# Optimization experiments

Hardware: AMD Instinct MI355X
Metric: run time of the kernel (lower is better)

## Reference

```python
import jax, jax.numpy as jnp
import numpy as np

B, S, H, NH = 2, 384, 768, 12
DPH = H // NH
SCALE = 1.0 / np.sqrt(DPH)


def _layer_norm(x, g, b, eps=1e-6):
    m = jnp.mean(x, axis=-1, keepdims=True)
    v = jnp.mean(jnp.square(x - m), axis=-1, keepdims=True)
    return (x - m) * jax.lax.rsqrt(v + eps) * g + b


def setup_inputs() -> dict:
    key = jax.random.key(0)
    ks = jax.random.split(key, 12)
    std = 0.02
    return {
        "hidden_states": jax.random.normal(ks[0], (B, S, H), jnp.float32),
        "attention_mask": jnp.ones((B, S), jnp.int32),
        "rel_pos_embedding": jax.random.normal(ks[1], (B, S, S, H), jnp.float32),
        "Wq": jax.random.normal(ks[2], (H, H), jnp.float32) * std,
        "bq": jnp.zeros((H,), jnp.float32),
        "Wk": jax.random.normal(ks[3], (H, H), jnp.float32) * std,
        "bk": jnp.zeros((H,), jnp.float32),
        "Wv": jax.random.normal(ks[4], (H, H), jnp.float32) * std,
        "bv": jnp.zeros((H,), jnp.float32),
        "Wr": jax.random.normal(ks[5], (H, H), jnp.float32) * std,
        "br": jnp.zeros((H,), jnp.float32),
        "u": jax.random.normal(ks[6], (NH, DPH), jnp.float32) * std,
        "v": jax.random.normal(ks[7], (NH, DPH), jnp.float32) * std,
        "Wf": jax.random.normal(ks[8], (H, H), jnp.float32) * std,
        "bf": jnp.zeros((H,), jnp.float32),
        "ln_g": jnp.ones((H,), jnp.float32),
        "ln_b": jnp.zeros((H,), jnp.float32),
    }


def reference(hidden_states, attention_mask, rel_pos_embedding,
              Wq, bq, Wk, bk, Wv, bv, Wr, br, u, v, Wf, bf, ln_g, ln_b):
    # projections (torch Linear: x @ W.T + b)
    def heads(x):  # [B,S,H] -> [B,NH,S,DPH]
        return x.reshape(B, S, NH, DPH).transpose(0, 2, 1, 3)
    q = heads(hidden_states @ Wq.T + bq)
    k = heads(hidden_states @ Wk.T + bk)
    val = heads(hidden_states @ Wv.T + bv)
    # relative embedding projection: [B,S,S,H] -> [B,S,S,NH,DPH]
    rel = (rel_pos_embedding @ Wr.T + br).reshape(B, S, S, NH, DPH)

    # Transformer-XL style decomposition
    AC = jnp.einsum('bhid,bhjd->bhij', q + u[None, :, None, :], k)
    Bp = jnp.einsum('bhid,bijhd->bhij', q, rel)
    Dp = jnp.einsum('hd,bijhd->bhij', v, rel)
    scores = (AC + Bp + Dp) * SCALE

    # 2-D mask -> [B,1,1,S]
    ext = (1.0 - attention_mask[:, None, None, :].astype(scores.dtype)) * (-1e18)
    probs = jax.nn.softmax(scores + ext, axis=-1)  # dropout is identity at eval

    ctx = jnp.einsum('bhij,bhjd->bhid', probs, val)
    ctx = ctx.transpose(0, 2, 1, 3).reshape(B, S, H)
    out = ctx @ Wf.T + bf
    return _layer_norm(out + hidden_states, ln_g, ln_b)
```

## Files before the change

kernel.cpp:

```cpp
#include <hip/hip_runtime.h>
#include <cstddef>
#include <cstdint>

static constexpr int BB   = 2;
static constexpr int SS   = 384;
static constexpr int HH   = 768;
static constexpr int NHD  = 12;
static constexpr int ROWS = BB * SS;
#define SCALE_F 0.125f

typedef __attribute__((ext_vector_type(8))) short short8;
typedef __attribute__((ext_vector_type(4))) float f32x4;

static __device__ __forceinline__ unsigned short f2bf(float x) {
    unsigned int b = __float_as_uint(x);
    b = (b + 0x7fffu + ((b >> 16) & 1u)) >> 16;
    return (unsigned short)b;
}
static __device__ __forceinline__ float bf2f(unsigned short u) {
    return __uint_as_float((unsigned int)u << 16);
}

__global__ __launch_bounds__(256) void k_tobf(const float* __restrict__ s0,
                                              const float* __restrict__ s1,
                                              const float* __restrict__ s2,
                                              const float* __restrict__ s3,
                                              const float* __restrict__ s4,
                                              const float* __restrict__ Wr,
                                              unsigned short* __restrict__ d0,
                                              unsigned short* __restrict__ d1,
                                              unsigned short* __restrict__ d2,
                                              unsigned short* __restrict__ d3,
                                              unsigned short* __restrict__ d4,
                                              unsigned short* __restrict__ WrT) {
    __shared__ float t[32][33];
    const int z = blockIdx.y;
    if (z < 5) {
        const float* s = (z == 0) ? s0 : (z == 1) ? s1 : (z == 2) ? s2 : (z == 3) ? s3 : s4;
        unsigned short* d = (z == 0) ? d0 : (z == 1) ? d1 : (z == 2) ? d2 : (z == 3) ? d3 : d4;
        const int tt = blockIdx.x * 256 + threadIdx.x;
        const float4 v = *(const float4*)&s[(size_t)tt * 4];
        ushort4 o;
        o.x = f2bf(v.x); o.y = f2bf(v.y); o.z = f2bf(v.z); o.w = f2bf(v.w);
        *(ushort4*)&d[(size_t)tt * 4] = o;
    } else {
        const int tile = blockIdx.x;
        const int tr_ = tile / 24, tc_ = tile % 24;
        const int r = threadIdx.x >> 3, c4 = (threadIdx.x & 7) * 4;
        const float4 v = *(const float4*)&Wr[(size_t)(tr_ * 32 + r) * HH + tc_ * 32 + c4];
        t[r][c4 + 0] = v.x; t[r][c4 + 1] = v.y; t[r][c4 + 2] = v.z; t[r][c4 + 3] = v.w;
        __syncthreads();
        ushort4 o;
        o.x = f2bf(t[c4 + 0][r]); o.y = f2bf(t[c4 + 1][r]);
        o.z = f2bf(t[c4 + 2][r]); o.w = f2bf(t[c4 + 3][r]);
        *(ushort4*)&WrT[(size_t)(tc_ * 32 + r) * HH + tr_ * 32 + c4] = o;
    }
}

__global__ __launch_bounds__(256) void k_gemm_qkv(const unsigned short* __restrict__ A,
                                                  const unsigned short* __restrict__ Wqb, const float* __restrict__ bq,
                                                  const unsigned short* __restrict__ Wkb, const float* __restrict__ bk,
                                                  const unsigned short* __restrict__ Wvb, const float* __restrict__ bv,
                                                  const float* __restrict__ uvec,
                                                  const float* __restrict__ vvec,
                                                  unsigned short* __restrict__ qu_b,
                                                  unsigned short* __restrict__ qv_b,
                                                  unsigned short* __restrict__ k_b,
                                                  unsigned short* __restrict__ vT_b) {
    const int z = blockIdx.z;
    const unsigned short* W = (z == 0) ? Wqb : (z == 1) ? Wkb : Wvb;
    const float* bias = (z == 0) ? bq : (z == 1) ? bk : bv;

    const int tid = threadIdx.x;
    const int wid = tid >> 6, lane = tid & 63;
    const int i0 = blockIdx.y * 64, o0 = blockIdx.x * 64;
    const int wr = (wid >> 1) * 32, wc = (wid & 1) * 32;
    const int lrow = lane & 15;
    const int kgrp = (lane >> 4) * 8;

    const unsigned short* Ar0 = A + (size_t)(i0 + wr + lrow) * HH + kgrp;
    const unsigned short* Ar1 = Ar0 + 16 * HH;
    const unsigned short* Wr0 = W + (size_t)(o0 + wc + lrow) * HH + kgrp;
    const unsigned short* Wr1 = Wr0 + 16 * HH;

    f32x4 acc00 = {0.f,0.f,0.f,0.f}, acc01 = {0.f,0.f,0.f,0.f};
    f32x4 acc10 = {0.f,0.f,0.f,0.f}, acc11 = {0.f,0.f,0.f,0.f};
#pragma unroll 4
    for (int k0 = 0; k0 < HH; k0 += 32) {
        const short8 a0 = *(const short8*)(Ar0 + k0);
        const short8 a1 = *(const short8*)(Ar1 + k0);
        const short8 b0 = *(const short8*)(Wr0 + k0);
        const short8 b1 = *(const short8*)(Wr1 + k0);
        acc00 = __builtin_amdgcn_mfma_f32_16x16x32_bf16(a0, b0, acc00, 0, 0, 0);
        acc01 = __builtin_amdgcn_mfma_f32_16x16x32_bf16(a0, b1, acc01, 0, 0, 0);
        acc10 = __builtin_amdgcn_mfma_f32_16x16x32_bf16(a1, b0, acc10, 0, 0, 0);
        acc11 = __builtin_amdgcn_mfma_f32_16x16x32_bf16(a1, b1, acc11, 0, 0, 0);
    }

    const int rbase = (lane >> 4) * 4;
#pragma unroll
    for (int tr = 0; tr < 2; tr++) {
#pragma unroll
        for (int tc = 0; tc < 2; tc++) {
            const f32x4 a = (tr == 0) ? ((tc == 0) ? acc00 : acc01)
                                      : ((tc == 0) ? acc10 : acc11);
            const int col = o0 + wc + tc * 16 + lrow;
            const float bvv = bias[col];
            if (z == 0) {
                const float uu = uvec[col], vv = vvec[col];
#pragma unroll
                for (int r = 0; r < 4; r++) {
                    const int row = i0 + wr + tr * 16 + rbase + r;
                    const float val = a[r] + bvv;
                    qu_b[(size_t)row * HH + col] = f2bf(val + uu);
                    qv_b[(size_t)row * HH + col] = f2bf(val + vv);
                }
            } else if (z == 1) {
#pragma unroll
                for (int r = 0; r < 4; r++) {
                    const int row = i0 + wr + tr * 16 + rbase + r;
                    k_b[(size_t)row * HH + col] = f2bf(a[r] + bvv);
                }
            } else {
                const int row0 = i0 + wr + tr * 16 + rbase;
                const int bb2 = row0 / SS;
                const int jj0 = row0 - bb2 * SS;
                const int h2 = col >> 6, d2 = col & 63;
                ushort4 o;
                o.x = f2bf(a[0] + bvv); o.y = f2bf(a[1] + bvv);
                o.z = f2bf(a[2] + bvv); o.w = f2bf(a[3] + bvv);
                *(ushort4*)&vT_b[((size_t)(bb2 * NHD + h2) * 64 + d2) * SS + jj0] = o;
            }
        }
    }
}

__global__ void k_cb(const unsigned short* __restrict__ qv,
                     const float* __restrict__ br, float* __restrict__ cb) {
    const int t = blockIdx.x * 256 + threadIdx.x;
    if (t >= ROWS * NHD) return;
    const int row = t / NHD, h = t - row * NHD;
    float s = 0.f;
    for (int d = 0; d < 64; d++)
        s = fmaf(bf2f(qv[(size_t)row * HH + h * 64 + d]), br[h * 64 + d], s);
    cb[t] = s;
}

__global__ __launch_bounds__(256) void k_uproj(const unsigned short* __restrict__ qv,
                                               const unsigned short* __restrict__ WrT,
                                               unsigned short* __restrict__ U) {
    const int h = blockIdx.z;
    const int e0 = blockIdx.x * 64, r0 = blockIdx.y * 64;
    const int tid = threadIdx.x;
    const int wid = tid >> 6, lane = tid & 63;
    const int wr = (wid >> 1) * 32, wc = (wid & 1) * 32;
    const int lrow = lane & 15;
    const int kgrp = (lane >> 4) * 8;

    const unsigned short* Ar0 = qv + (size_t)(r0 + wr + lrow) * HH + h * 64 + kgrp;
    const unsigned short* Ar1 = Ar0 + 16 * HH;
    const unsigned short* Br0 = WrT + (size_t)(e0 + wc + lrow) * HH + h * 64 + kgrp;
    const unsigned short* Br1 = Br0 + 16 * HH;

    f32x4 acc00 = {0.f,0.f,0.f,0.f}, acc01 = {0.f,0.f,0.f,0.f};
    f32x4 acc10 = {0.f,0.f,0.f,0.f}, acc11 = {0.f,0.f,0.f,0.f};
#pragma unroll
    for (int k0 = 0; k0 < 64; k0 += 32) {
        const short8 a0 = *(const short8*)(Ar0 + k0);
        const short8 a1 = *(const short8*)(Ar1 + k0);
        const short8 b0 = *(const short8*)(Br0 + k0);
        const short8 b1 = *(const short8*)(Br1 + k0);
        acc00 = __builtin_amdgcn_mfma_f32_16x16x32_bf16(a0, b0, acc00, 0, 0, 0);
        acc01 = __builtin_amdgcn_mfma_f32_16x16x32_bf16(a0, b1, acc01, 0, 0, 0);
        acc10 = __builtin_amdgcn_mfma_f32_16x16x32_bf16(a1, b0, acc10, 0, 0, 0);
        acc11 = __builtin_amdgcn_mfma_f32_16x16x32_bf16(a1, b1, acc11, 0, 0, 0);
    }

    const int rbase = (lane >> 4) * 4;
#pragma unroll
    for (int tr = 0; tr < 2; tr++) {
#pragma unroll
        for (int tc = 0; tc < 2; tc++) {
            const f32x4 a = (tr == 0) ? ((tc == 0) ? acc00 : acc01)
                                      : ((tc == 0) ? acc10 : acc11);
            const int e = e0 + wc + tc * 16 + lrow;
#pragma unroll
            for (int r = 0; r < 4; r++) {
                const int row = r0 + wr + tr * 16 + rbase + r;
                U[(size_t)row * (NHD * HH) + (size_t)h * HH + e] = f2bf(a[r]);
            }
        }
    }
}

__global__ __launch_bounds__(256) void k_ac(const unsigned short* __restrict__ qu,
                                            const unsigned short* __restrict__ kb,
                                            const float* __restrict__ cb,
                                            float* __restrict__ sc) {
    const int bh = blockIdx.z;
    const int b = bh / NHD, h = bh - b * NHD;
    const int i0 = blockIdx.y * 64, j0 = blockIdx.x * 64;
    const int tid = threadIdx.x;
    const int wid = tid >> 6, lane = tid & 63;
    const int wr = (wid >> 1) * 32, wc = (wid & 1) * 32;
    const int lrow = lane & 15;
    const int kgrp = (lane >> 4) * 8;

    const unsigned short* Ar0 = qu + (size_t)(b * SS + i0 + wr + lrow) * HH + h * 64 + kgrp;
    const unsigned short* Ar1 = Ar0 + 16 * HH;
    const unsigned short* Br0 = kb + (size_t)(b * SS + j0 + wc + lrow) * HH + h * 64 + kgrp;
    const unsigned short* Br1 = Br0 + 16 * HH;

    f32x4 acc00 = {0.f,0.f,0.f,0.f}, acc01 = {0.f,0.f,0.f,0.f};
    f32x4 acc10 = {0.f,0.f,0.f,0.f}, acc11 = {0.f,0.f,0.f,0.f};
#pragma unroll
    for (int k0 = 0; k0 < 64; k0 += 32) {
        const short8 a0 = *(const short8*)(Ar0 + k0);
        const short8 a1 = *(const short8*)(Ar1 + k0);
        const short8 b0 = *(const short8*)(Br0 + k0);
        const short8 b1 = *(const short8*)(Br1 + k0);
        acc00 = __builtin_amdgcn_mfma_f32_16x16x32_bf16(a0, b0, acc00, 0, 0, 0);
        acc01 = __builtin_amdgcn_mfma_f32_16x16x32_bf16(a0, b1, acc01, 0, 0, 0);
        acc10 = __builtin_amdgcn_mfma_f32_16x16x32_bf16(a1, b0, acc10, 0, 0, 0);
        acc11 = __builtin_amdgcn_mfma_f32_16x16x32_bf16(a1, b1, acc11, 0, 0, 0);
    }

    const int rbase = (lane >> 4) * 4;
#pragma unroll
    for (int tr = 0; tr < 2; tr++) {
#pragma unroll
        for (int tc = 0; tc < 2; tc++) {
            const f32x4 a = (tr == 0) ? ((tc == 0) ? acc00 : acc01)
                                      : ((tc == 0) ? acc10 : acc11);
            const int j = j0 + wc + tc * 16 + lrow;
#pragma unroll
            for (int r = 0; r < 4; r++) {
                const int i = i0 + wr + tr * 16 + rbase + r;
                const float cbr = cb[(b * SS + i) * NHD + h];
                sc[((size_t)(b * SS + i) * NHD + h) * SS + j] = a[r] + cbr;
            }
        }
    }
}

__global__ __launch_bounds__(256) void k_bd(const float* __restrict__ rpe,
                                            const unsigned short* __restrict__ U,
                                            const int* __restrict__ mask,
                                            const float* __restrict__ scin,
                                            unsigned short* __restrict__ Pb) {
    const int i = blockIdx.x;
    const int b = blockIdx.y;
    const int row = b * SS + i;
    const int tid = threadIdx.x;

    __shared__ unsigned short Ul[NHD * HH];
    __shared__ float sc[NHD][392];
    __shared__ float extl[SS];

    const float* plane = scin + (size_t)row * NHD * SS;
    unsigned short* pplane = Pb + (size_t)row * NHD * SS;

    {
        const uint4* Ur = (const uint4*)(U + (size_t)row * NHD * HH);
        uint4* Uld = (uint4*)Ul;
        for (int t = tid; t < NHD * HH / 8; t += 256) Uld[t] = Ur[t];
        for (int t = tid; t < NHD * 96; t += 256) {
            const int h = t / 96, c4 = (t - h * 96) << 2;
            *(float4*)&sc[h][c4] = *(const float4*)&plane[h * SS + c4];
        }
        for (int t = tid; t < SS; t += 256)
            extl[t] = (1.0f - (float)mask[b * SS + t]) * (-1e18f);
    }
    __syncthreads();

    const int wave = tid >> 6;
    const int lane = tid & 63;

    {
        const int jsub = lane >> 3;
        const int elane = lane & 7;
        const float* rrow = rpe + (size_t)row * SS * HH;

        for (int g = wave; g < 12; g += 4) {
            const int jbase = g * 32 + jsub;
            const float* rp0 = rrow + (size_t)jbase * HH + (elane << 2);
            float acc[4][NHD] = {};
#pragma unroll 2
            for (int ec = 0; ec < 24; ec++) {
                const int eo = ec << 5;
                const float4 t0 = *(const float4*)(rp0 + eo);
                const float4 t1 = *(const float4*)(rp0 + eo + 8 * HH);
                const float4 t2 = *(const float4*)(rp0 + eo + 16 * HH);
                const float4 t3 = *(const float4*)(rp0 + eo + 24 * HH);
                const float rb[4][4] = {{t0.x, t0.y, t0.z, t0.w},
                                        {t1.x, t1.y, t1.z, t1.w},
                                        {t2.x, t2.y, t2.z, t2.w},
                                        {t3.x, t3.y, t3.z, t3.w}};
                const int uo = eo + (elane << 2);
#pragma unroll
                for (int h = 0; h < NHD; h++) {
                    const uint2 w2 = *(const uint2*)&Ul[h * HH + uo];
                    float ub[4];
                    ub[0] = __uint_as_float(w2.x << 16);
                    ub[1] = __uint_as_float(w2.x & 0xffff0000u);
                    ub[2] = __uint_as_float(w2.y << 16);
                    ub[3] = __uint_as_float(w2.y & 0xffff0000u);
#pragma unroll
                    for (int rr = 0; rr < 4; rr++)
#pragma unroll
                        for (int c = 0; c < 4; c++)
                            acc[rr][h] = fmaf(rb[rr][c], ub[c], acc[rr][h]);
                }
            }
#pragma unroll
            for (int rr = 0; rr < 4; rr++)
#pragma unroll
                for (int h = 0; h < NHD; h++) {
                    float a = acc[rr][h];
                    a += __shfl_xor(a, 1);
                    a += __shfl_xor(a, 2);
                    a += __shfl_xor(a, 4);
                    acc[rr][h] = a;
                }
            if (elane == 0) {
#pragma unroll
                for (int rr = 0; rr < 4; rr++) {
                    const int j = jbase + (rr << 3);
#pragma unroll
                    for (int h = 0; h < NHD; h++)
                        sc[h][j] += acc[rr][h];
                }
            }
        }
    }
    __syncthreads();

    {
        for (int h = wave; h < NHD; h += 4) {
            float vbuf[6];
            float m = -1e30f;
#pragma unroll
            for (int t2 = 0; t2 < 6; t2++) {
                vbuf[t2] = sc[h][lane + t2 * 64] * SCALE_F + extl[lane + t2 * 64];
                m = fmaxf(m, vbuf[t2]);
            }
#pragma unroll
            for (int off = 1; off < 64; off <<= 1) m = fmaxf(m, __shfl_xor(m, off));
            float ssum = 0.f;
#pragma unroll
            for (int t2 = 0; t2 < 6; t2++) {
                const float e = __expf(vbuf[t2] - m);
                vbuf[t2] = e;
                ssum += e;
            }
#pragma unroll
            for (int off = 1; off < 64; off <<= 1) ssum += __shfl_xor(ssum, off);
            const float inv = 1.0f / ssum;
#pragma unroll
            for (int t2 = 0; t2 < 6; t2++)
                pplane[h * SS + lane + t2 * 64] = f2bf(vbuf[t2] * inv);
        }
    }
}

__global__ __launch_bounds__(256) void k_pv(const unsigned short* __restrict__ Pb,
                                            const unsigned short* __restrict__ vTb,
                                            unsigned short* __restrict__ ctxb) {
    const int bh = blockIdx.y;
    const int b = bh / NHD, h = bh - b * NHD;
    const int i0 = blockIdx.x * 64;
    const int tid = threadIdx.x;
    const int wid = tid >> 6, lane = tid & 63;
    const int wr = (wid >> 1) * 32, wc = (wid & 1) * 32;
    const int lrow = lane & 15;
    const int kgrp = (lane >> 4) * 8;

    const unsigned short* Ar0 = Pb + ((size_t)(b * SS + i0 + wr + lrow) * NHD + h) * SS + kgrp;
    const unsigned short* Ar1 = Ar0 + (size_t)16 * NHD * SS;
    const unsigned short* Br0 = vTb + ((size_t)(b * NHD + h) * 64 + wc + lrow) * SS + kgrp;
    const unsigned short* Br1 = Br0 + 16 * SS;

    f32x4 acc00 = {0.f,0.f,0.f,0.f}, acc01 = {0.f,0.f,0.f,0.f};
    f32x4 acc10 = {0.f,0.f,0.f,0.f}, acc11 = {0.f,0.f,0.f,0.f};
#pragma unroll 4
    for (int k0 = 0; k0 < SS; k0 += 32) {
        const short8 a0 = *(const short8*)(Ar0 + k0);
        const short8 a1 = *(const short8*)(Ar1 + k0);
        const short8 b0 = *(const short8*)(Br0 + k0);
        const short8 b1 = *(const short8*)(Br1 + k0);
        acc00 = __builtin_amdgcn_mfma_f32_16x16x32_bf16(a0, b0, acc00, 0, 0, 0);
        acc01 = __builtin_amdgcn_mfma_f32_16x16x32_bf16(a0, b1, acc01, 0, 0, 0);
        acc10 = __builtin_amdgcn_mfma_f32_16x16x32_bf16(a1, b0, acc10, 0, 0, 0);
        acc11 = __builtin_amdgcn_mfma_f32_16x16x32_bf16(a1, b1, acc11, 0, 0, 0);
    }

    const int rbase = (lane >> 4) * 4;
#pragma unroll
    for (int tr = 0; tr < 2; tr++) {
#pragma unroll
        for (int tc = 0; tc < 2; tc++) {
            const f32x4 a = (tr == 0) ? ((tc == 0) ? acc00 : acc01)
                                      : ((tc == 0) ? acc10 : acc11);
            const int d = wc + tc * 16 + lrow;
#pragma unroll
            for (int r = 0; r < 4; r++) {
                const int row = b * SS + i0 + wr + tr * 16 + rbase + r;
                ctxb[(size_t)row * HH + h * 64 + d] = f2bf(a[r]);
            }
        }
    }
}

__global__ __launch_bounds__(256) void k_gemm_out(const unsigned short* __restrict__ A,
                                                  const unsigned short* __restrict__ W,
                                                  const float* __restrict__ bias,
                                                  const float* __restrict__ addsrc,
                                                  float* __restrict__ C) {
    const int tid = threadIdx.x;
    const int wid = tid >> 6, lane = tid & 63;
    const int i0 = blockIdx.y * 64, o0 = blockIdx.x * 64;
    const int wr = (wid >> 1) * 32, wc = (wid & 1) * 32;
    const int lrow = lane & 15;
    const int kgrp = (lane >> 4) * 8;

    const unsigned short* Ar0 = A + (size_t)(i0 + wr + lrow) * HH + kgrp;
    const unsigned short* Ar1 = Ar0 + 16 * HH;
    const unsigned short* Wr0 = W + (size_t)(o0 + wc + lrow) * HH + kgrp;
    const unsigned short* Wr1 = Wr0 + 16 * HH;

    f32x4 acc00 = {0.f,0.f,0.f,0.f}, acc01 = {0.f,0.f,0.f,0.f};
    f32x4 acc10 = {0.f,0.f,0.f,0.f}, acc11 = {0.f,0.f,0.f,0.f};
#pragma unroll 4
    for (int k0 = 0; k0 < HH; k0 += 32) {
        const short8 a0 = *(const short8*)(Ar0 + k0);
        const short8 a1 = *(const short8*)(Ar1 + k0);
        const short8 b0 = *(const short8*)(Wr0 + k0);
        const short8 b1 = *(const short8*)(Wr1 + k0);
        acc00 = __builtin_amdgcn_mfma_f32_16x16x32_bf16(a0, b0, acc00, 0, 0, 0);
        acc01 = __builtin_amdgcn_mfma_f32_16x16x32_bf16(a0, b1, acc01, 0, 0, 0);
        acc10 = __builtin_amdgcn_mfma_f32_16x16x32_bf16(a1, b0, acc10, 0, 0, 0);
        acc11 = __builtin_amdgcn_mfma_f32_16x16x32_bf16(a1, b1, acc11, 0, 0, 0);
    }

    const int rbase = (lane >> 4) * 4;
#pragma unroll
    for (int tr = 0; tr < 2; tr++) {
#pragma unroll
        for (int tc = 0; tc < 2; tc++) {
            const f32x4 a = (tr == 0) ? ((tc == 0) ? acc00 : acc01)
                                      : ((tc == 0) ? acc10 : acc11);
            const int col = o0 + wc + tc * 16 + lrow;
            const float bv = bias[col];
#pragma unroll
            for (int r = 0; r < 4; r++) {
                const int row = i0 + wr + tr * 16 + rbase + r;
                C[(size_t)row * HH + col] = a[r] + bv + addsrc[(size_t)row * HH + col];
            }
        }
    }
}

__global__ __launch_bounds__(256) void k_ln(const float* __restrict__ x,
                                            const float* __restrict__ g,
                                            const float* __restrict__ bta,
                                            float* __restrict__ o) {
    const int row = blockIdx.x;
    const int tid = threadIdx.x;
    const float* xr = x + (size_t)row * HH;
    __shared__ float red[4];
    const float v0 = xr[tid], v1 = xr[tid + 256], v2 = xr[tid + 512];
    float s = v0 + v1 + v2;
#pragma unroll
    for (int off = 1; off < 64; off <<= 1) s += __shfl_xor(s, off);
    if ((tid & 63) == 0) red[tid >> 6] = s;
    __syncthreads();
    const float mean = (red[0] + red[1] + red[2] + red[3]) * (1.0f / 768.0f);
    const float d0 = v0 - mean, d1 = v1 - mean, d2 = v2 - mean;
    float sq = d0 * d0 + d1 * d1 + d2 * d2;
#pragma unroll
    for (int off = 1; off < 64; off <<= 1) sq += __shfl_xor(sq, off);
    __syncthreads();
    if ((tid & 63) == 0) red[tid >> 6] = sq;
    __syncthreads();
    const float var = (red[0] + red[1] + red[2] + red[3]) * (1.0f / 768.0f);
    const float inv = rsqrtf(var + 1e-6f);
    o[(size_t)row * HH + tid]       = d0 * inv * g[tid]       + bta[tid];
    o[(size_t)row * HH + tid + 256] = d1 * inv * g[tid + 256] + bta[tid + 256];
    o[(size_t)row * HH + tid + 512] = d2 * inv * g[tid + 512] + bta[tid + 512];
}

extern "C" void kernel_launch(void* const* d_in, const int* in_sizes, int n_in,
                              void* d_out, int out_size, void* d_ws, size_t ws_size,
                              hipStream_t stream) {
    (void)in_sizes; (void)n_in; (void)out_size; (void)ws_size;
    const float* hs   = (const float*)d_in[0];
    const int*   mask = (const int*)d_in[1];
    const float* rpe  = (const float*)d_in[2];
    const float* Wq = (const float*)d_in[3];  const float* bq = (const float*)d_in[4];
    const float* Wk = (const float*)d_in[5];  const float* bk = (const float*)d_in[6];
    const float* Wv = (const float*)d_in[7];  const float* bv = (const float*)d_in[8];
    const float* Wr = (const float*)d_in[9];  const float* br = (const float*)d_in[10];
    const float* u  = (const float*)d_in[11]; const float* v  = (const float*)d_in[12];
    const float* Wf = (const float*)d_in[13]; const float* bf = (const float*)d_in[14];
    const float* lng = (const float*)d_in[15]; const float* lnb = (const float*)d_in[16];
    float* out = (float*)d_out;

    const size_t MAT = (size_t)ROWS * HH;
    float* wsf     = (float*)d_ws;
    float* lnin_ws = wsf;
    float* sc_ws   = lnin_ws + MAT;
    float* cb_ws   = sc_ws + (size_t)ROWS * NHD * SS;
    unsigned short* U_ws  = (unsigned short*)(cb_ws + (size_t)ROWS * NHD);
    unsigned short* hs_b  = U_ws + (size_t)ROWS * NHD * HH;
    unsigned short* Wq_b  = hs_b + MAT;
    unsigned short* Wk_b  = Wq_b + MAT;
    unsigned short* Wv_b  = Wk_b + MAT;
    unsigned short* Wf_b  = Wv_b + MAT;
    unsigned short* WrT_b = Wf_b + MAT;
    unsigned short* qu_b  = WrT_b + MAT;
    unsigned short* qv_b  = qu_b + MAT;
    unsigned short* k_b   = qv_b + MAT;
    unsigned short* vT_b  = k_b + MAT;
    unsigned short* ctx_b = vT_b + MAT;
    unsigned short* P_b   = ctx_b + MAT;

    k_tobf<<<dim3(576, 6), 256, 0, stream>>>(hs, Wq, Wk, Wv, Wf, Wr,
                                             hs_b, Wq_b, Wk_b, Wv_b, Wf_b, WrT_b);
    k_gemm_qkv<<<dim3(12, 12, 3), 256, 0, stream>>>(hs_b, Wq_b, bq, Wk_b, bk, Wv_b, bv,
                                                    u, v, qu_b, qv_b, k_b, vT_b);
    k_cb<<<dim3(36), 256, 0, stream>>>(qv_b, br, cb_ws);
    k_uproj<<<dim3(12, 12, 12), 256, 0, stream>>>(qv_b, WrT_b, U_ws);
    k_ac<<<dim3(6, 6, 24), 256, 0, stream>>>(qu_b, k_b, cb_ws, sc_ws);
    k_bd<<<dim3(SS, BB), 256, 0, stream>>>(rpe, U_ws, mask, sc_ws, P_b);
    k_pv<<<dim3(6, 24), 256, 0, stream>>>(P_b, vT_b, ctx_b);
    k_gemm_out<<<dim3(12, 12), 256, 0, stream>>>(ctx_b, Wf_b, bf, hs, lnin_ws);
    k_ln<<<dim3(768), 256, 0, stream>>>(lnin_ws, lng, lnb, out);
}
```

Before: 262.8 us.

## Merge cb, uproj and AC kernels into one launch; restructure rel-pos streaming

Folds the three small mid-stage kernels (cb bias dot, U projection, AC scores) into a single grid-partitioned launch. The cb term is now computed per tile into shared memory and is no longer written to a workspace buffer. This removes two launches and the cb round trip, at the cost of some recomputation of cb per j-tile. Separately, the k_bd inner loop changes so each wave processes one j row at a time with contiguous 128-float strides along the embedding, instead of four rows 8 apart. This changes the memory access pattern over the large rel_pos_embedding stream and lowers accumulator register pressure.

Measured after the change: 272.0 us. 1.03x slower.

```diff
diff --git a/kernel.cpp b/kernel.cpp
--- a/kernel.cpp
+++ b/kernel.cpp
@@ -135,109 +135,108 @@
     }
 }
 
-__global__ void k_cb(const unsigned short* __restrict__ qv,
-                     const float* __restrict__ br, float* __restrict__ cb) {
-    const int t = blockIdx.x * 256 + threadIdx.x;
-    if (t >= ROWS * NHD) return;
-    const int row = t / NHD, h = t - row * NHD;
-    float s = 0.f;
-    for (int d = 0; d < 64; d++)
-        s = fmaf(bf2f(qv[(size_t)row * HH + h * 64 + d]), br[h * 64 + d], s);
-    cb[t] = s;
-}
-
-__global__ __launch_bounds__(256) void k_uproj(const unsigned short* __restrict__ qv,
-                                               const unsigned short* __restrict__ WrT,
-                                               unsigned short* __restrict__ U) {
-    const int h = blockIdx.z;
-    const int e0 = blockIdx.x * 64, r0 = blockIdx.y * 64;
+__global__ __launch_bounds__(256) void k_mid(const unsigned short* __restrict__ qv,
+                                             const unsigned short* __restrict__ WrT,
+                                             const unsigned short* __restrict__ qu,
+                                             const unsigned short* __restrict__ kb,
+                                             const float* __restrict__ br,
+                                             unsigned short* __restrict__ U,
+                                             float* __restrict__ sc) {
+    __shared__ float cbl[64];
+    const int bx = blockIdx.x;
     const int tid = threadIdx.x;
     const int wid = tid >> 6, lane = tid & 63;
     const int wr = (wid >> 1) * 32, wc = (wid & 1) * 32;
     const int lrow = lane & 15;
     const int kgrp = (lane >> 4) * 8;
-
-    const unsigned short* Ar0 = qv + (size_t)(r0 + wr + lrow) * HH + h * 64 + kgrp;
-    const unsigned short* Ar1 = Ar0 + 16 * HH;
-    const unsigned short* Br0 = WrT + (size_t)(e0 + wc + lrow) * HH + h * 64 + kgrp;
-    const unsigned short* Br1 = Br0 + 16 * HH;
-
-    f32x4 acc00 = {0.f,0.f,0.f,0.f}, acc01 = {0.f,0.f,0.f,0.f};
-    f32x4 acc10 = {0.f,0.f,0.f,0.f}, acc11 = {0.f,0.f,0.f,0.f};
-#pragma unroll
-    for (int k0 = 0; k0 < 64; k0 += 32) {
-        const short8 a0 = *(const short8*)(Ar0 + k0);
-        const short8 a1 = *(const short8*)(Ar1 + k0);
-        const short8 b0 = *(const short8*)(Br0 + k0);
-        const short8 b1 = *(const short8*)(Br1 + k0);
-        acc00 = __builtin_amdgcn_mfma_f32_16x16x32_bf16(a0, b0, acc00, 0, 0, 0);
-        acc01 = __builtin_amdgcn_mfma_f32_16x16x32_bf16(a0, b1, acc01, 0, 0, 0);
-        acc10 = __builtin_amdgcn_mfma_f32_16x16x32_bf16(a1, b0, acc10, 0, 0, 0);
-        acc11 = __builtin_amdgcn_mfma_f32_16x16x32_bf16(a1, b1, acc11, 0, 0, 0);
-    }
-
     const int rbase = (lane >> 4) * 4;
-#pragma unroll
-    for (int tr = 0; tr < 2; tr++) {
-#pragma unroll
-        for (int tc = 0; tc < 2; tc++) {
-            const f32x4 a = (tr == 0) ? ((tc == 0) ? acc00 : acc01)
-                                      : ((tc == 0) ? acc10 : acc11);
-            const int e = e0 + wc + tc * 16 + lrow;
-#pragma unroll
-            for (int r = 0; r < 4; r++) {
-                const int row = r0 + wr + tr * 16 + rbase + r;
-                U[(size_t)row * (NHD * HH) + (size_t)h * HH + e] = f2bf(a[r]);
-            }
-        }
-    }
-}
-
-__global__ __launch_bounds__(256) void k_ac(const unsigned short* __restrict__ qu,
-                                            const unsigned short* __restrict__ kb,
-                                            const float* __restrict__ cb,
-                                            float* __restrict__ sc) {
-    const int bh = blockIdx.z;
-    const int b = bh / NHD, h = bh - b * NHD;
-    const int i0 = blockIdx.y * 64, j0 = blockIdx.x * 64;
-    const int tid = threadIdx.x;
-    const int wid = tid >> 6, lane = tid & 63;
-    const int wr = (wid >> 1) * 32, wc = (wid & 1) * 32;
-    const int lrow = lane & 15;
-    const int kgrp = (lane >> 4) * 8;
-
-    const unsigned short* Ar0 = qu + (size_t)(b * SS + i0 + wr + lrow) * HH + h * 64 + kgrp;
-    const unsigned short* Ar1 = Ar0 + 16 * HH;
-    const unsigned short* Br0 = kb + (size_t)(b * SS + j0 + wc + lrow) * HH + h * 64 + kgrp;
-    const unsigned short* Br1 = Br0 + 16 * HH;
-
-    f32x4 acc00 = {0.f,0.f,0.f,0.f}, acc01 = {0.f,0.f,0.f,0.f};
-    f32x4 acc10 = {0.f,0.f,0.f,0.f}, acc11 = {0.f,0.f,0.f,0.f};
-#pragma unroll
-    for (int k0 = 0; k0 < 64; k0 += 32) {
-        const short8 a0 = *(const short8*)(Ar0 + k0);
-        const short8 a1 = *(const short8*)(Ar1 + k0);
-        const short8 b0 = *(const short8*)(Br0 + k0);
-        const short8 b1 = *(const short8*)(Br1 + k0);
-        acc00 = __builtin_amdgcn_mfma_f32_16x16x32_bf16(a0, b0, acc00, 0, 0, 0);
-        acc01 = __builtin_amdgcn_mfma_f32_16x16x32_bf16(a0, b1, acc01, 0, 0, 0);
-        acc10 = __builtin_amdgcn_mfma_f32_16x16x32_bf16(a1, b0, acc10, 0, 0, 0);
-        acc11 = __builtin_amdgcn_mfma_f32_16x16x32_bf16(a1, b1, acc11, 0, 0, 0);
-    }
-
-    const int rbase = (lane >> 4) * 4;
-#pragma unroll
-    for (int tr = 0; tr < 2; tr++) {
-#pragma unroll
-        for (int tc = 0; tc < 2; tc++) {
-            const f32x4 a = (tr == 0) ? ((tc == 0) ? acc00 : acc01)
-                                      : ((tc == 0) ? acc10 : acc11);
-            const int j = j0 + wc + tc * 16 + lrow;
-#pragma unroll
-            for (int r = 0; r < 4; r++) {
-                const int i = i0 + wr + tr * 16 + rbase + r;
-                const float cbr = cb[(b * SS + i) * NHD + h];
-                sc[((size_t)(b * SS + i) * NHD + h) * SS + j] = a[r] + cbr;
+
+    if (bx < 1728) {
+        const int h = bx / 144;
+        const int r0 = ((bx / 12) % 12) * 64, e0 = (bx % 12) * 64;
+
+        const unsigned short* Ar0 = qv + (size_t)(r0 + wr + lrow) * HH + h * 64 + kgrp;
+        const unsigned short* Ar1 = Ar0 + 16 * HH;
+        const unsigned short* Br0 = WrT + (size_t)(e0 + wc + lrow) * HH + h * 64 + kgrp;
+        const unsigned short* Br1 = Br0 + 16 * HH;
+
+        f32x4 acc00 = {0.f,0.f,0.f,0.f}, acc01 = {0.f,0.f,0.f,0.f};
+        f32x4 acc10 = {0.f,0.f,0.f,0.f}, acc11 = {0.f,0.f,0.f,0.f};
+#pragma unroll
+        for (int k0 = 0; k0 < 64; k0 += 32) {
+            const short8 a0 = *(const short8*)(Ar0 + k0);
+            const short8 a1 = *(const short8*)(Ar1 + k0);
+            const short8 b0 = *(const short8*)(Br0 + k0);
+            const short8 b1 = *(const short8*)(Br1 + k0);
+            acc00 = __builtin_amdgcn_mfma_f32_16x16x32_bf16(a0, b0, acc00, 0, 0, 0);
+            acc01 = __builtin_amdgcn_mfma_f32_16x16x32_bf16(a0, b1, acc01, 0, 0, 0);
+            acc10 = __builtin_amdgcn_mfma_f32_16x16x32_bf16(a1, b0, acc10, 0, 0, 0);
+            acc11 = __builtin_amdgcn_mfma_f32_16x16x32_bf16(a1, b1, acc11, 0, 0, 0);
+        }
+#pragma unroll
+        for (int tr = 0; tr < 2; tr++) {
+#pragma unroll
+            for (int tc = 0; tc < 2; tc++) {
+                const f32x4 a = (tr == 0) ? ((tc == 0) ? acc00 : acc01)
+                                          : ((tc == 0) ? acc10 : acc11);
+                const int e = e0 + wc + tc * 16 + lrow;
+#pragma unroll
+                for (int r = 0; r < 4; r++) {
+                    const int row = r0 + wr + tr * 16 + rbase + r;
+                    U[(size_t)row * (NHD * HH) + (size_t)h * HH + e] = f2bf(a[r]);
+                }
+            }
+        }
+    } else {
+        const int idx = bx - 1728;
+        const int j0 = (idx % 6) * 64, i0 = ((idx / 6) % 6) * 64;
+        const int bh = idx / 36;
+        const int b = bh / NHD, h = bh - b * NHD;
+
+        {
+            const int r = tid >> 2, seg = tid & 3;
+            const unsigned short* qrow = qv + (size_t)(b * SS + i0 + r) * HH + h * 64 + seg * 16;
+            const float* brp = br + h * 64 + seg * 16;
+            float p = 0.f;
+#pragma unroll
+            for (int d = 0; d < 16; d++)
+                p = fmaf(bf2f(qrow[d]), brp[d], p);
+            p += __shfl_xor(p, 1);
+            p += __shfl_xor(p, 2);
+            if (seg == 0) cbl[r] = p;
+        }
+        __syncthreads();
+
+        const unsigned short* Ar0 = qu + (size_t)(b * SS + i0 + wr + lrow) * HH + h * 64 + kgrp;
+        const unsigned short* Ar1 = Ar0 + 16 * HH;
+        const unsigned short* Br0 = kb + (size_t)(b * SS + j0 + wc + lrow) * HH + h * 64 + kgrp;
+        const unsigned short* Br1 = Br0 + 16 * HH;
+
+        f32x4 acc00 = {0.f,0.f,0.f,0.f}, acc01 = {0.f,0.f,0.f,0.f};
+        f32x4 acc10 = {0.f,0.f,0.f,0.f}, acc11 = {0.f,0.f,0.f,0.f};
+#pragma unroll
+        for (int k0 = 0; k0 < 64; k0 += 32) {
+            const short8 a0 = *(const short8*)(Ar0 + k0);
+            const short8 a1 = *(const short8*)(Ar1 + k0);
+            const short8 b0 = *(const short8*)(Br0 + k0);
+            const short8 b1 = *(const short8*)(Br1 + k0);
+            acc00 = __builtin_amdgcn_mfma_f32_16x16x32_bf16(a0, b0, acc00, 0, 0, 0);
+            acc01 = __builtin_amdgcn_mfma_f32_16x16x32_bf16(a0, b1, acc01, 0, 0, 0);
+            acc10 = __builtin_amdgcn_mfma_f32_16x16x32_bf16(a1, b0, acc10, 0, 0, 0);
+            acc11 = __builtin_amdgcn_mfma_f32_16x16x32_bf16(a1, b1, acc11, 0, 0, 0);
+        }
+#pragma unroll
+        for (int tr = 0; tr < 2; tr++) {
+#pragma unroll
+            for (int tc = 0; tc < 2; tc++) {
+                const f32x4 a = (tr == 0) ? ((tc == 0) ? acc00 : acc01)
+                                          : ((tc == 0) ? acc10 : acc11);
+                const int j = j0 + wc + tc * 16 + lrow;
+#pragma unroll
+                for (int r = 0; r < 4; r++) {
+                    const int ii = i0 + wr + tr * 16 + rbase + r;
+                    sc[((size_t)(b * SS + ii) * NHD + h) * SS + j] = a[r] + cbl[ii - i0];
+                }
             }
         }
     }
@@ -281,17 +280,17 @@
         const int elane = lane & 7;
         const float* rrow = rpe + (size_t)row * SS * HH;
 
-        for (int g = wave; g < 12; g += 4) {
-            const int jbase = g * 32 + jsub;
-            const float* rp0 = rrow + (size_t)jbase * HH + (elane << 2);
-            float acc[4][NHD] = {};
+        for (int g = wave; g < 48; g += 4) {
+            const int j = (g << 3) + jsub;
+            const float* rp0 = rrow + (size_t)j * HH + (elane << 2);
+            float acc[NHD] = {};
 #pragma unroll 2
-            for (int ec = 0; ec < 24; ec++) {
-                const int eo = ec << 5;
+            for (int ec = 0; ec < 6; ec++) {
+                const int eo = ec * 128;
                 const float4 t0 = *(const float4*)(rp0 + eo);
-                const float4 t1 = *(const float4*)(rp0 + eo + 8 * HH);
-                const float4 t2 = *(const float4*)(rp0 + eo + 16 * HH);
-                const float4 t3 = *(const float4*)(rp0 + eo + 24 * HH);
+                const float4 t1 = *(const float4*)(rp0 + eo + 32);
+                const float4 t2 = *(const float4*)(rp0 + eo + 64);
+                const float4 t3 = *(const float4*)(rp0 + eo + 96);
                 const float rb[4][4] = {{t0.x, t0.y, t0.z, t0.w},
                                         {t1.x, t1.y, t1.z, t1.w},
                                         {t2.x, t2.y, t2.z, t2.w},
@@ -299,37 +298,28 @@
                 const int uo = eo + (elane << 2);
 #pragma unroll
                 for (int h = 0; h < NHD; h++) {
-                    const uint2 w2 = *(const uint2*)&Ul[h * HH + uo];
-                    float ub[4];
-                    ub[0] = __uint_as_float(w2.x << 16);
-                    ub[1] = __uint_as_float(w2.x & 0xffff0000u);
-                    ub[2] = __uint_as_float(w2.y << 16);
-                    ub[3] = __uint_as_float(w2.y & 0xffff0000u);
-#pragma unroll
-                    for (int rr = 0; rr < 4; rr++)
-#pragma unroll
-                        for (int c = 0; c < 4; c++)
-                            acc[rr][h] = fmaf(rb[rr][c], ub[c], acc[rr][h]);
+                    const unsigned short* up = &Ul[h * HH + uo];
+#pragma unroll
+                    for (int c = 0; c < 4; c++) {
+                        const uint2 w2 = *(const uint2*)(up + c * 32);
+                        const float u0 = __uint_as_float(w2.x << 16);
+                        const float u1 = __uint_as_float(w2.x & 0xffff0000u);
+                        const float u2 = __uint_as_float(w2.y << 16);
+                        const float u3 = __uint_as_float(w2.y & 0xffff0000u);
+                        acc[h] = fmaf(rb[c][0], u0, acc[h]);
+                        acc[h] = fmaf(rb[c][1], u1, acc[h]);
+                        acc[h] = fmaf(rb[c][2], u2, acc[h]);
+                        acc[h] = fmaf(rb[c][3], u3, acc[h]);
+                    }
                 }
             }
 #pragma unroll
-            for (int rr = 0; rr < 4; rr++)
-#pragma unroll
-                for (int h = 0; h < NHD; h++) {
-                    float a = acc[rr][h];
-                    a += __shfl_xor(a, 1);
-                    a += __shfl_xor(a, 2);
-                    a += __shfl_xor(a, 4);
-                    acc[rr][h] = a;
-                }
-            if (elane == 0) {
-#pragma unroll
-                for (int rr = 0; rr < 4; rr++) {
-                    const int j = jbase + (rr << 3);
-#pragma unroll
-                    for (int h = 0; h < NHD; h++)
-                        sc[h][j] += acc[rr][h];
-                }
+            for (int h = 0; h < NHD; h++) {
+                float a = acc[h];
+                a += __shfl_xor(a, 1);
+                a += __shfl_xor(a, 2);
+                a += __shfl_xor(a, 4);
+                if (elane == 0) sc[h][j] += a;
             }
         }
     }
@@ -509,8 +499,7 @@
     float* wsf     = (float*)d_ws;
     float* lnin_ws = wsf;
     float* sc_ws   = lnin_ws + MAT;
-    float* cb_ws   = sc_ws + (size_t)ROWS * NHD * SS;
-    unsigned short* U_ws  = (unsigned short*)(cb_ws + (size_t)ROWS * NHD);
+    unsigned short* U_ws  = (unsigned short*)(sc_ws + (size_t)ROWS * NHD * SS);
     unsigned short* hs_b  = U_ws + (size_t)ROWS * NHD * HH;
     unsigned short* Wq_b  = hs_b + MAT;
     unsigned short* Wk_b  = Wq_b + MAT;
@@ -528,9 +517,7 @@
                                              hs_b, Wq_b, Wk_b, Wv_b, Wf_b, WrT_b);
     k_gemm_qkv<<<dim3(12, 12, 3), 256, 0, stream>>>(hs_b, Wq_b, bq, Wk_b, bk, Wv_b, bv,
                                                     u, v, qu_b, qv_b, k_b, vT_b);
-    k_cb<<<dim3(36), 256, 0, stream>>>(qv_b, br, cb_ws);
-    k_uproj<<<dim3(12, 12, 12), 256, 0, stream>>>(qv_b, WrT_b, U_ws);
-    k_ac<<<dim3(6, 6, 24), 256, 0, stream>>>(qu_b, k_b, cb_ws, sc_ws);
+    k_mid<<<dim3(2592), 256, 0, stream>>>(qv_b, WrT_b, qu_b, k_b, br, U_ws, sc_ws);
     k_bd<<<dim3(SS, BB), 256, 0, stream>>>(rpe, U_ws, mask, sc_ws, P_b);
     k_pv<<<dim3(6, 24), 256, 0, stream>>>(P_b, vT_b, ctx_b);
     k_gemm_out<<<dim3(12, 12), 256, 0, stream>>>(ctx_b, Wf_b, bf, hs, lnin_ws);
```
